# Optimization experiments

Hardware: AMD Instinct MI355X
Metric: run time of the kernel (lower is better)

## Reference

```python
import jax, jax.numpy as jnp
import numpy as np


def _maxpool2x2(t):
    # t: [B, C, H, W] -> [B, C, H//2, W//2]
    B, C, H, W = t.shape
    return t.reshape(B, C, H // 2, 2, W // 2, 2).max(axis=(3, 5))


def setup_inputs() -> dict:
    key = jax.random.key(0)
    ks = jax.random.split(key, 6)
    B, C, H, W = 2, 64, 128, 128
    x = jax.random.normal(ks[0], (B, C, H, W), dtype=jnp.float32)
    w_theta = jax.random.normal(ks[1], (C // 8, C), dtype=jnp.float32) * 0.05
    w_phi = jax.random.normal(ks[2], (C // 8, C), dtype=jnp.float32) * 0.05
    w_g = jax.random.normal(ks[3], (C // 2, C), dtype=jnp.float32) * 0.05
    w_o = jax.random.normal(ks[4], (C, C // 2), dtype=jnp.float32) * 0.05
    gamma = jnp.ones((1,), dtype=jnp.float32)
    return {"x": x, "w_theta": w_theta, "w_phi": w_phi, "w_g": w_g,
            "w_o": w_o, "gamma": gamma}


def reference(x, w_theta, w_phi, w_g, w_o, gamma):
    B, C, H, W = x.shape
    N = H * W            # query length
    M = (H // 2) * (W // 2)  # downsampled key/value length

    # conv1x1 projections (kernel_size=1 == per-pixel matmul over channels)
    theta = jnp.einsum('bchw,oc->bohw', x, w_theta).reshape(B, C // 8, N)
    phi = jnp.einsum('bchw,oc->bohw', x, w_phi)
    phi = _maxpool2x2(phi).reshape(B, C // 8, M)

    # attention: [B, N, M], unscaled dot product + softmax over keys
    attn = jax.nn.softmax(jnp.einsum('bdn,bdm->bnm', theta, phi), axis=-1)

    g = jnp.einsum('bchw,oc->bohw', x, w_g)
    g = _maxpool2x2(g).reshape(B, C // 2, M)

    attn_g = jnp.einsum('bcm,bnm->bcn', g, attn).reshape(B, C // 2, H, W)
    attn_g = jnp.einsum('bchw,oc->bohw', attn_g, w_o)
    return x + gamma * attn_g
```

## Files before the change

### kernel.cpp

```cpp
#include <hip/hip_runtime.h>

#define BB 2
#define CC 64
#define HH 128
#define WW 128
#define NN (HH*WW)
#define MM ((HH/2)*(WW/2))
#define CV 32
#define LOG2E 1.44269504088896f

typedef __attribute__((ext_vector_type(8))) short bf16x8;
typedef __attribute__((ext_vector_type(4))) float f32x4;
typedef unsigned int uint32;

union U8 { bf16x8 v; uint32 u[4]; };

__device__ __forceinline__ short f2bf(float f) {
    union { float f; unsigned u; } v; v.f = f;
    unsigned u = v.u + 0x7fffu + ((v.u >> 16) & 1u);
    return (short)(u >> 16);
}
__device__ __forceinline__ uint32 pack2bf(float lo, float hi) {
    return (uint32)(unsigned short)f2bf(lo) | ((uint32)(unsigned short)f2bf(hi) << 16);
}
__device__ __forceinline__ uint32 packperm(float lo, float hi) {
    union { float f; uint32 u; } a, b; a.f = lo; b.f = hi;
    return __builtin_amdgcn_perm(b.u, a.u, 0x07060302u);
}
__device__ __forceinline__ void gl_lds16(const short* g, short* l) {
    __builtin_amdgcn_global_load_lds(
        (const __attribute__((address_space(1))) void*)g,
        (__attribute__((address_space(3))) void*)l, 16, 0, 0);
}

__global__ __launch_bounds__(256, 4) void proj_kernel(
    const float* __restrict__ x, const float* __restrict__ wt,
    const float* __restrict__ wp, const float* __restrict__ wg,
    short* __restrict__ Qb, short* __restrict__ Kb, short* __restrict__ Vt)
{
    __shared__ float plds[8192];
    __shared__ float phi_lds[512];
    int tid = threadIdx.x;
    int px = tid & 63, part = tid >> 6;
    int sb = blockIdx.x >> 2, cq = blockIdx.x & 3;
    int b = blockIdx.y;
    int row = px >> 5, col = cq*32 + (px & 31);
    int n = (2*sb + row)*WW + col;
    int wbase = __builtin_amdgcn_readfirstlane(part*16);

    float xv[16];
    #pragma unroll
    for (int i = 0; i < 16; ++i)
        xv[i] = x[((b*CC + part*16 + i) << 14) + n];

    {
        float po[16];
        #pragma unroll
        for (int o = 0; o < 8; ++o) {
            float a = 0.f;
            #pragma unroll
            for (int i = 0; i < 16; ++i) a += wt[o*64 + wbase + i]*xv[i];
            po[o] = a;
        }
        #pragma unroll
        for (int o = 0; o < 8; ++o) {
            float a = 0.f;
            #pragma unroll
            for (int i = 0; i < 16; ++i) a += wp[o*64 + wbase + i]*xv[i];
            po[8+o] = a;
        }
        #pragma unroll
        for (int o = 0; o < 16; ++o) plds[(o*4 + part)*64 + px] = po[o];
        __syncthreads();
        int og = tid >> 6;
        float sm[4];
        #pragma unroll
        for (int j = 0; j < 4; ++j) {
            int o = og*4 + j;
            sm[j] = (plds[(o*4+0)*64+px] + plds[(o*4+1)*64+px])
                  + (plds[(o*4+2)*64+px] + plds[(o*4+3)*64+px]);
        }
        if (og < 2) {
            uint2 val;
            val.x = pack2bf(sm[0]*LOG2E, sm[1]*LOG2E);
            val.y = pack2bf(sm[2]*LOG2E, sm[3]*LOG2E);
            ((uint2*)Qb)[(b*NN + n)*2 + og] = val;
        } else {
            #pragma unroll
            for (int j = 0; j < 4; ++j)
                phi_lds[((og-2)*4 + j)*64 + px] = sm[j];
        }
        __syncthreads();
        if (tid < 128) {
            int mm = tid & 15, ch = tid >> 4;
            int p00 = 2*mm, p01 = p00+1, p10 = 32+2*mm, p11 = p10+1;
            float mx = fmaxf(fmaxf(phi_lds[ch*64+p00], phi_lds[ch*64+p01]),
                             fmaxf(phi_lds[ch*64+p10], phi_lds[ch*64+p11]));
            int m = sb*64 + cq*16 + mm;
            Kb[(b*MM + m)*8 + ch] = f2bf(mx);
        }
    }

    {
        float po[32];
        #pragma unroll
        for (int o = 0; o < 32; ++o) {
            float a = 0.f;
            #pragma unroll
            for (int i = 0; i < 16; ++i) a += wg[o*64 + wbase + i]*xv[i];
            po[o] = a;
        }
        #pragma unroll
        for (int o = 0; o < 32; ++o) plds[(o*4 + part)*64 + px] = po[o];
        __syncthreads();
        int og = tid >> 6;
        float sm[8];
        #pragma unroll
        for (int j = 0; j < 8; ++j) {
            int o = og*8 + j;
            sm[j] = (plds[(o*4+0)*64+px] + plds[(o*4+1)*64+px])
                  + (plds[(o*4+2)*64+px] + plds[(o*4+3)*64+px]);
        }
        __syncthreads();
        #pragma unroll
        for (int j = 0; j < 8; ++j)
            plds[(og*8 + j)*64 + px] = sm[j];
        __syncthreads();
        int mm = tid & 15, chb = tid >> 4;
        int p00 = 2*mm, p01 = p00+1, p10 = 32+2*mm, p11 = p10+1;
        int w64 = cq*16 + mm;
        int hh = w64 >> 5, w = w64 & 31;
        int slot = ((w >> 2) & 3)*8 + (w & 3) + ((w >> 4) << 2);
        int pos64 = hh*32 + slot;
        #pragma unroll
        for (int j = 0; j < 2; ++j) {
            int ch = chb*2 + j;
            float mx = fmaxf(fmaxf(plds[ch*64+p00], plds[ch*64+p01]),
                             fmaxf(plds[ch*64+p10], plds[ch*64+p11]));
            int colv = (pos64 >> 3) ^ (ch & 7);
            Vt[(b*CV + ch)*MM + sb*64 + colv*8 + (pos64 & 7)] = f2bf(mx);
        }
    }
}

__global__ __launch_bounds__(512, 4) void attn_kernel(
    const short* __restrict__ Qb, const short* __restrict__ Kb,
    const short* __restrict__ Vt, const float* __restrict__ x,
    const float* __restrict__ wo, const float* __restrict__ gamma,
    float* __restrict__ out)
{
    __shared__ short ldsK[2][4][512];
    __shared__ short ldsV[2][4][2048];
    __shared__ float comb[2][2][576];
    int tid = threadIdx.x;
    int wave = tid >> 6, lane = tid & 63;
    int quad = lane >> 4, c15 = lane & 15, sw = c15 & 7;
    int qtr = wave >> 1, qpair = wave & 1;
    int blk = blockIdx.x;
    int b = blk >> 8;
    int qblk = (blk & 255)*64;
    int q0 = qblk + qpair*32;

    const f32x4 zero4 = {0.f, 0.f, 0.f, 0.f};
    bf16x8 zero8 = (bf16x8)0;
    U8 ones; ones.u[0] = ones.u[1] = ones.u[2] = ones.u[3] = 0x3F803F80u;

    bf16x8 bq0 = (quad == 0) ? ((const bf16x8*)Qb)[b*NN + q0 + c15]      : zero8;
    bf16x8 bq1 = (quad == 0) ? ((const bf16x8*)Qb)[b*NN + q0 + 16 + c15] : zero8;

    const short* vsrcA = Vt + ((size_t)(b*CV + 16*qpair + (lane >> 3)))*MM
                       + qtr*1024 + (lane & 7)*8;
    const short* vsrcB = vsrcA + 8*MM;
    const short* ksrc  = Kb + (size_t)b*MM*8 + (qtr*1024 + lane)*8;
    short* vdstA[2] = { &ldsV[0][qtr][qpair*1024 + lane*8],
                        &ldsV[1][qtr][qpair*1024 + lane*8] };
    short* vdstB[2] = { vdstA[0] + 512, vdstA[1] + 512 };
    short* kdst[2]  = { &ldsK[0][qtr][lane*8], &ldsK[1][qtr][lane*8] };

    {
        gl_lds16(vsrcA, vdstA[0]);
        gl_lds16(vsrcB, vdstB[0]);
        if (qpair == 0) gl_lds16(ksrc, kdst[0]);
    }
    __syncthreads();

    f32x4 D0A = zero4, D1A = zero4, DlA = zero4;
    f32x4 D0B = zero4, D1B = zero4, DlB = zero4;

    for (int sc = 0; sc < 16; ++sc) {
        int scn = (sc + 1 > 15) ? 15 : sc + 1;
        int nb = (sc + 1) & 1;
        gl_lds16(vsrcA + scn*64, vdstA[nb]);
        gl_lds16(vsrcB + scn*64, vdstB[nb]);
        if (qpair == 0) gl_lds16(ksrc + scn*512, kdst[nb]);

        const short* bk = ldsK[sc & 1][qtr];
        const short* bv = ldsV[sc & 1][qtr];
        #pragma unroll
        for (int h = 0; h < 2; ++h) {
            bf16x8 kf0 = *(const bf16x8*)(bk + (h*32 + c15)*8);
            bf16x8 kf1 = *(const bf16x8*)(bk + (h*32 + 16 + c15)*8);
            int col8 = ((h*4 + quad) ^ sw)*8;
            bf16x8 a0 = *(const bf16x8*)(bv + c15*64 + col8);
            bf16x8 a1 = *(const bf16x8*)(bv + (16 + c15)*64 + col8);
            __builtin_amdgcn_s_setprio(1);
            f32x4 s0A = __builtin_amdgcn_mfma_f32_16x16x32_bf16(kf0, bq0, zero4, 0, 0, 0);
            f32x4 s1A = __builtin_amdgcn_mfma_f32_16x16x32_bf16(kf1, bq0, zero4, 0, 0, 0);
            f32x4 s0B = __builtin_amdgcn_mfma_f32_16x16x32_bf16(kf0, bq1, zero4, 0, 0, 0);
            f32x4 s1B = __builtin_amdgcn_mfma_f32_16x16x32_bf16(kf1, bq1, zero4, 0, 0, 0);
            __builtin_amdgcn_s_setprio(0);
            U8 bpA, bpB;
            bpA.u[0] = packperm(__builtin_amdgcn_exp2f(s0A[0]), __builtin_amdgcn_exp2f(s0A[1]));
            bpA.u[1] = packperm(__builtin_amdgcn_exp2f(s0A[2]), __builtin_amdgcn_exp2f(s0A[3]));
            bpA.u[2] = packperm(__builtin_amdgcn_exp2f(s1A[0]), __builtin_amdgcn_exp2f(s1A[1]));
            bpA.u[3] = packperm(__builtin_amdgcn_exp2f(s1A[2]), __builtin_amdgcn_exp2f(s1A[3]));
            bpB.u[0] = packperm(__builtin_amdgcn_exp2f(s0B[0]), __builtin_amdgcn_exp2f(s0B[1]));
            bpB.u[1] = packperm(__builtin_amdgcn_exp2f(s0B[2]), __builtin_amdgcn_exp2f(s0B[3]));
            bpB.u[2] = packperm(__builtin_amdgcn_exp2f(s1B[0]), __builtin_amdgcn_exp2f(s1B[1]));
            bpB.u[3] = packperm(__builtin_amdgcn_exp2f(s1B[2]), __builtin_amdgcn_exp2f(s1B[3]));
            __builtin_amdgcn_s_setprio(1);
            D0A = __builtin_amdgcn_mfma_f32_16x16x32_bf16(a0, bpA.v, D0A, 0, 0, 0);
            D1A = __builtin_amdgcn_mfma_f32_16x16x32_bf16(a1, bpA.v, D1A, 0, 0, 0);
            DlA = __builtin_amdgcn_mfma_f32_16x16x32_bf16(ones.v, bpA.v, DlA, 0, 0, 0);
            D0B = __builtin_amdgcn_mfma_f32_16x16x32_bf16(a0, bpB.v, D0B, 0, 0, 0);
            D1B = __builtin_amdgcn_mfma_f32_16x16x32_bf16(a1, bpB.v, D1B, 0, 0, 0);
            DlB = __builtin_amdgcn_mfma_f32_16x16x32_bf16(ones.v, bpB.v, DlB, 0, 0, 0);
            __builtin_amdgcn_s_setprio(0);
        }
        __syncthreads();
    }

    #pragma unroll
    for (int r = 1; r < 4; ++r) {
        if (qtr == r) {
            float* cA = &comb[qpair][0][lane*9];
            cA[0]=D0A[0]; cA[1]=D0A[1]; cA[2]=D0A[2]; cA[3]=D0A[3];
            cA[4]=D1A[0]; cA[5]=D1A[1]; cA[6]=D1A[2]; cA[7]=D1A[3];
            cA[8]=DlA[0];
            float* cB = &comb[qpair][1][lane*9];
            cB[0]=D0B[0]; cB[1]=D0B[1]; cB[2]=D0B[2]; cB[3]=D0B[3];
            cB[4]=D1B[0]; cB[5]=D1B[1]; cB[6]=D1B[2]; cB[7]=D1B[3];
            cB[8]=DlB[0];
        }
        __syncthreads();
        if (qtr == 0) {
            const float* cA = &comb[qpair][0][lane*9];
            D0A[0]+=cA[0]; D0A[1]+=cA[1]; D0A[2]+=cA[2]; D0A[3]+=cA[3];
            D1A[0]+=cA[4]; D1A[1]+=cA[5]; D1A[2]+=cA[6]; D1A[3]+=cA[7];
            DlA[0]+=cA[8];
            const float* cB = &comb[qpair][1][lane*9];
            D0B[0]+=cB[0]; D0B[1]+=cB[1]; D0B[2]+=cB[2]; D0B[3]+=cB[3];
            D1B[0]+=cB[4]; D1B[1]+=cB[5]; D1B[2]+=cB[6]; D1B[3]+=cB[7];
            DlB[0]+=cB[8];
        }
        __syncthreads();
    }
    if (qtr != 0) return;

    float rlA = 1.0f / DlA[0];
    float rlB = 1.0f / DlB[0];
    U8 ByA, ByB;
    ByA.u[0] = pack2bf(D0A[0]*rlA, D0A[1]*rlA); ByA.u[1] = pack2bf(D0A[2]*rlA, D0A[3]*rlA);
    ByA.u[2] = pack2bf(D1A[0]*rlA, D1A[1]*rlA); ByA.u[3] = pack2bf(D1A[2]*rlA, D1A[3]*rlA);
    ByB.u[0] = pack2bf(D0B[0]*rlB, D0B[1]*rlB); ByB.u[1] = pack2bf(D0B[2]*rlB, D0B[3]*rlB);
    ByB.u[2] = pack2bf(D1B[0]*rlB, D1B[1]*rlB); ByB.u[3] = pack2bf(D1B[2]*rlB, D1B[3]*rlB);

    float gam = gamma[0];
    #pragma unroll
    for (int t = 0; t < 4; ++t) {
        int co = t*16 + c15;
        float4 wlo = *(const float4*)(wo + co*32 + quad*4);
        float4 whi = *(const float4*)(wo + co*32 + 16 + quad*4);
        U8 aw;
        aw.u[0] = pack2bf(wlo.x, wlo.y); aw.u[1] = pack2bf(wlo.z, wlo.w);
        aw.u[2] = pack2bf(whi.x, whi.y); aw.u[3] = pack2bf(whi.z, whi.w);
        f32x4 oA = __builtin_amdgcn_mfma_f32_16x16x32_bf16(aw.v, ByA.v, zero4, 0, 0, 0);
        f32x4 oB = __builtin_amdgcn_mfma_f32_16x16x32_bf16(aw.v, ByB.v, zero4, 0, 0, 0);
        #pragma unroll
        for (int r2 = 0; r2 < 4; ++r2) {
            int co_r = t*16 + quad*4 + r2;
            int base = ((b*CC + co_r) << 14) + q0 + c15;
            out[base]      = x[base]      + gam*oA[r2];
            out[base + 16] = x[base + 16] + gam*oB[r2];
        }
    }
}

extern "C" void kernel_launch(void* const* d_in, const int* in_sizes, int n_in,
                              void* d_out, int out_size, void* d_ws, size_t ws_size,
                              hipStream_t stream) {
    const float* x     = (const float*)d_in[0];
    const float* wt    = (const float*)d_in[1];
    const float* wp    = (const float*)d_in[2];
    const float* wg    = (const float*)d_in[3];
    const float* wo    = (const float*)d_in[4];
    const float* gamma = (const float*)d_in[5];
    float* out = (float*)d_out;

    char* ws = (char*)d_ws;
    short* Qb = (short*)(ws);
    short* Kb = (short*)(ws + 524288);
    short* Vt = (short*)(ws + 655360);

    dim3 g1(256, BB);
    proj_kernel<<<g1, 256, 0, stream>>>(x, wt, wp, wg, Qb, Kb, Vt);
    attn_kernel<<<BB*NN/64, 512, 0, stream>>>(Qb, Kb, Vt, x, wo, gamma, out);
}
```

Before: 101.4 us.

## Load K/V fragments directly from global into registers, drop LDS staging

The attention kernel no longer stages K and V tiles through double-buffered LDS with global_load_lds and per-chunk barriers. Each wave now reads its MFMA fragments straight from global memory (L2/L1 cached) into registers, prefetching the next iteration one step ahead. This removes the LDS traffic and the 16 __syncthreads per block. In exchange, the two query-pair waves load the same K/V data redundantly, the loads are less coalesced 16-byte per-lane reads, and latency hiding rests on a single-step register prefetch.

```diff
diff --git a/kernel.cpp b/kernel.cpp
--- a/kernel.cpp
+++ b/kernel.cpp
@@ -26,11 +26,6 @@
 __device__ __forceinline__ uint32 packperm(float lo, float hi) {
     union { float f; uint32 u; } a, b; a.f = lo; b.f = hi;
     return __builtin_amdgcn_perm(b.u, a.u, 0x07060302u);
-}
-__device__ __forceinline__ void gl_lds16(const short* g, short* l) {
-    __builtin_amdgcn_global_load_lds(
-        (const __attribute__((address_space(1))) void*)g,
-        (__attribute__((address_space(3))) void*)l, 16, 0, 0);
 }
 
 __global__ __launch_bounds__(256, 4) void proj_kernel(
@@ -149,8 +144,6 @@
     const float* __restrict__ wo, const float* __restrict__ gamma,
     float* __restrict__ out)
 {
-    __shared__ short ldsK[2][4][512];
-    __shared__ short ldsV[2][4][2048];
     __shared__ float comb[2][2][576];
     int tid = threadIdx.x;
     int wave = tid >> 6, lane = tid & 63;
@@ -168,66 +161,57 @@
     bf16x8 bq0 = (quad == 0) ? ((const bf16x8*)Qb)[b*NN + q0 + c15]      : zero8;
     bf16x8 bq1 = (quad == 0) ? ((const bf16x8*)Qb)[b*NN + q0 + 16 + c15] : zero8;
 
-    const short* vsrcA = Vt + ((size_t)(b*CV + 16*qpair + (lane >> 3)))*MM
-                       + qtr*1024 + (lane & 7)*8;
-    const short* vsrcB = vsrcA + 8*MM;
-    const short* ksrc  = Kb + (size_t)b*MM*8 + (qtr*1024 + lane)*8;
-    short* vdstA[2] = { &ldsV[0][qtr][qpair*1024 + lane*8],
-                        &ldsV[1][qtr][qpair*1024 + lane*8] };
-    short* vdstB[2] = { vdstA[0] + 512, vdstA[1] + 512 };
-    short* kdst[2]  = { &ldsK[0][qtr][lane*8], &ldsK[1][qtr][lane*8] };
-
-    {
-        gl_lds16(vsrcA, vdstA[0]);
-        gl_lds16(vsrcB, vdstB[0]);
-        if (qpair == 0) gl_lds16(ksrc, kdst[0]);
-    }
-    __syncthreads();
+    const short* kptr  = Kb + ((size_t)b*MM + qtr*1024)*8;
+    const short* v0ptr = Vt + ((size_t)(b*CV + c15))*MM + qtr*1024;
+    const short* v1ptr = v0ptr + 16*MM;
 
     f32x4 D0A = zero4, D1A = zero4, DlA = zero4;
     f32x4 D0B = zero4, D1B = zero4, DlB = zero4;
 
-    for (int sc = 0; sc < 16; ++sc) {
-        int scn = (sc + 1 > 15) ? 15 : sc + 1;
-        int nb = (sc + 1) & 1;
-        gl_lds16(vsrcA + scn*64, vdstA[nb]);
-        gl_lds16(vsrcB + scn*64, vdstB[nb]);
-        if (qpair == 0) gl_lds16(ksrc + scn*512, kdst[nb]);
-
-        const short* bk = ldsK[sc & 1][qtr];
-        const short* bv = ldsV[sc & 1][qtr];
-        #pragma unroll
-        for (int h = 0; h < 2; ++h) {
-            bf16x8 kf0 = *(const bf16x8*)(bk + (h*32 + c15)*8);
-            bf16x8 kf1 = *(const bf16x8*)(bk + (h*32 + 16 + c15)*8);
-            int col8 = ((h*4 + quad) ^ sw)*8;
-            bf16x8 a0 = *(const bf16x8*)(bv + c15*64 + col8);
-            bf16x8 a1 = *(const bf16x8*)(bv + (16 + c15)*64 + col8);
-            __builtin_amdgcn_s_setprio(1);
-            f32x4 s0A = __builtin_amdgcn_mfma_f32_16x16x32_bf16(kf0, bq0, zero4, 0, 0, 0);
-            f32x4 s1A = __builtin_amdgcn_mfma_f32_16x16x32_bf16(kf1, bq0, zero4, 0, 0, 0);
-            f32x4 s0B = __builtin_amdgcn_mfma_f32_16x16x32_bf16(kf0, bq1, zero4, 0, 0, 0);
-            f32x4 s1B = __builtin_amdgcn_mfma_f32_16x16x32_bf16(kf1, bq1, zero4, 0, 0, 0);
-            __builtin_amdgcn_s_setprio(0);
-            U8 bpA, bpB;
-            bpA.u[0] = packperm(__builtin_amdgcn_exp2f(s0A[0]), __builtin_amdgcn_exp2f(s0A[1]));
-            bpA.u[1] = packperm(__builtin_amdgcn_exp2f(s0A[2]), __builtin_amdgcn_exp2f(s0A[3]));
-            bpA.u[2] = packperm(__builtin_amdgcn_exp2f(s1A[0]), __builtin_amdgcn_exp2f(s1A[1]));
-            bpA.u[3] = packperm(__builtin_amdgcn_exp2f(s1A[2]), __builtin_amdgcn_exp2f(s1A[3]));
-            bpB.u[0] = packperm(__builtin_amdgcn_exp2f(s0B[0]), __builtin_amdgcn_exp2f(s0B[1]));
-            bpB.u[1] = packperm(__builtin_amdgcn_exp2f(s0B[2]), __builtin_amdgcn_exp2f(s0B[3]));
-            bpB.u[2] = packperm(__builtin_amdgcn_exp2f(s1B[0]), __builtin_amdgcn_exp2f(s1B[1]));
-            bpB.u[3] = packperm(__builtin_amdgcn_exp2f(s1B[2]), __builtin_amdgcn_exp2f(s1B[3]));
-            __builtin_amdgcn_s_setprio(1);
-            D0A = __builtin_amdgcn_mfma_f32_16x16x32_bf16(a0, bpA.v, D0A, 0, 0, 0);
-            D1A = __builtin_amdgcn_mfma_f32_16x16x32_bf16(a1, bpA.v, D1A, 0, 0, 0);
-            DlA = __builtin_amdgcn_mfma_f32_16x16x32_bf16(ones.v, bpA.v, DlA, 0, 0, 0);
-            D0B = __builtin_amdgcn_mfma_f32_16x16x32_bf16(a0, bpB.v, D0B, 0, 0, 0);
-            D1B = __builtin_amdgcn_mfma_f32_16x16x32_bf16(a1, bpB.v, D1B, 0, 0, 0);
-            DlB = __builtin_amdgcn_mfma_f32_16x16x32_bf16(ones.v, bpB.v, DlB, 0, 0, 0);
-            __builtin_amdgcn_s_setprio(0);
-        }
-        __syncthreads();
+    bf16x8 kf0, kf1, a0, a1;
+    {
+        kf0 = *(const bf16x8*)(kptr + c15*8);
+        kf1 = *(const bf16x8*)(kptr + (16 + c15)*8);
+        int col8 = (quad ^ sw)*8;
+        a0 = *(const bf16x8*)(v0ptr + col8);
+        a1 = *(const bf16x8*)(v1ptr + col8);
+    }
+
+    #pragma unroll 4
+    for (int it = 0; it < 32; ++it) {
+        int nit = (it < 31) ? it + 1 : 31;
+        int nsc = nit >> 1, nh = nit & 1;
+        bf16x8 nk0 = *(const bf16x8*)(kptr + (nsc*64 + nh*32 + c15)*8);
+        bf16x8 nk1 = *(const bf16x8*)(kptr + (nsc*64 + nh*32 + 16 + c15)*8);
+        int ncol8 = ((nh*4 + quad) ^ sw)*8;
+        bf16x8 nv0 = *(const bf16x8*)(v0ptr + nsc*64 + ncol8);
+        bf16x8 nv1 = *(const bf16x8*)(v1ptr + nsc*64 + ncol8);
+
+        __builtin_amdgcn_s_setprio(1);
+        f32x4 s0A = __builtin_amdgcn_mfma_f32_16x16x32_bf16(kf0, bq0, zero4, 0, 0, 0);
+        f32x4 s1A = __builtin_amdgcn_mfma_f32_16x16x32_bf16(kf1, bq0, zero4, 0, 0, 0);
+        f32x4 s0B = __builtin_amdgcn_mfma_f32_16x16x32_bf16(kf0, bq1, zero4, 0, 0, 0);
+        f32x4 s1B = __builtin_amdgcn_mfma_f32_16x16x32_bf16(kf1, bq1, zero4, 0, 0, 0);
+        __builtin_amdgcn_s_setprio(0);
+        U8 bpA, bpB;
+        bpA.u[0] = packperm(__builtin_amdgcn_exp2f(s0A[0]), __builtin_amdgcn_exp2f(s0A[1]));
+        bpA.u[1] = packperm(__builtin_amdgcn_exp2f(s0A[2]), __builtin_amdgcn_exp2f(s0A[3]));
+        bpA.u[2] = packperm(__builtin_amdgcn_exp2f(s1A[0]), __builtin_amdgcn_exp2f(s1A[1]));
+        bpA.u[3] = packperm(__builtin_amdgcn_exp2f(s1A[2]), __builtin_amdgcn_exp2f(s1A[3]));
+        bpB.u[0] = packperm(__builtin_amdgcn_exp2f(s0B[0]), __builtin_amdgcn_exp2f(s0B[1]));
+        bpB.u[1] = packperm(__builtin_amdgcn_exp2f(s0B[2]), __builtin_amdgcn_exp2f(s0B[3]));
+        bpB.u[2] = packperm(__builtin_amdgcn_exp2f(s1B[0]), __builtin_amdgcn_exp2f(s1B[1]));
+        bpB.u[3] = packperm(__builtin_amdgcn_exp2f(s1B[2]), __builtin_amdgcn_exp2f(s1B[3]));
+        __builtin_amdgcn_s_setprio(1);
+        D0A = __builtin_amdgcn_mfma_f32_16x16x32_bf16(a0, bpA.v, D0A, 0, 0, 0);
+        D1A = __builtin_amdgcn_mfma_f32_16x16x32_bf16(a1, bpA.v, D1A, 0, 0, 0);
+        DlA = __builtin_amdgcn_mfma_f32_16x16x32_bf16(ones.v, bpA.v, DlA, 0, 0, 0);
+        D0B = __builtin_amdgcn_mfma_f32_16x16x32_bf16(a0, bpB.v, D0B, 0, 0, 0);
+        D1B = __builtin_amdgcn_mfma_f32_16x16x32_bf16(a1, bpB.v, D1B, 0, 0, 0);
+        DlB = __builtin_amdgcn_mfma_f32_16x16x32_bf16(ones.v, bpB.v, DlB, 0, 0, 0);
+        __builtin_amdgcn_s_setprio(0);
+
+        kf0 = nk0; kf1 = nk1; a0 = nv0; a1 = nv1;
     }
 
     #pragma unroll
```

New measurement: 105.0 us. 3.6% more time.
